# Kernel optimization log

Hardware: AMD Instinct MI355X
Metric: run time of the kernel (lower is better)

## Reference

```python
import jax, jax.numpy as jnp
import numpy as np

NUM_HEADS = 12


def setup_inputs() -> dict:
    key = jax.random.key(0)
    ks = jax.random.split(key, 8)
    B, D, H, W, C = 4, 8, 14, 14, 768
    hd = C // NUM_HEADS
    return {
        "x": jax.random.normal(ks[0], (B, D, H, W, C), jnp.float32),
        "qkv_w": jax.random.normal(ks[1], (C, 3 * C), jnp.float32) * (C ** -0.5),
        "qkv_b": jax.random.normal(ks[2], (3 * C,), jnp.float32) * 0.02,
        "proj_w": jax.random.normal(ks[3], (C, C), jnp.float32) * (C ** -0.5),
        "proj_b": jax.random.normal(ks[4], (C,), jnp.float32) * 0.02,
        "rel_pos_d": jax.random.normal(ks[5], (2 * D - 1, hd), jnp.float32) * 0.02,
        "rel_pos_h": jax.random.normal(ks[6], (2 * H - 1, hd), jnp.float32) * 0.02,
        "rel_pos_w": jax.random.normal(ks[7], (2 * W - 1, hd), jnp.float32) * 0.02,
    }


def _rel_table(table, n):
    # q_size == k_size == n; relative coords in [0, 2n-2]
    idx = jnp.arange(n)[:, None] - jnp.arange(n)[None, :] + (n - 1)
    return table[idx]  # [n, n, head_dim]


def reference(x, qkv_w, qkv_b, proj_w, proj_b, rel_pos_d, rel_pos_h, rel_pos_w):
    B, D, H, W, C = x.shape
    hd = C // NUM_HEADS
    scale = hd ** -0.5
    N = D * H * W
    BH = B * NUM_HEADS

    qkv = x @ qkv_w + qkv_b  # [B,D,H,W,3C]
    qkv = qkv.reshape(B, N, 3, NUM_HEADS, hd).transpose(2, 0, 3, 1, 4).reshape(3, BH, N, hd)
    q, k, v = qkv[0], qkv[1], qkv[2]

    attn = jnp.einsum('bnc,bmc->bnm', q * scale, k)  # [BH, N, N]

    # decomposed 3D relative position bias
    Rd = _rel_table(rel_pos_d, D)  # [D,D,hd]
    Rh = _rel_table(rel_pos_h, H)  # [H,H,hd]
    Rw = _rel_table(rel_pos_w, W)  # [W,W,hd]
    r_q = q.reshape(BH, D, H, W, hd)
    rel_d = jnp.einsum('bdhwc,dkc->bdhwk', r_q, Rd)  # [BH,D,H,W,D]
    rel_h = jnp.einsum('bdhwc,hkc->bdhwk', r_q, Rh)  # [BH,D,H,W,H]
    rel_w = jnp.einsum('bdhwc,wkc->bdhwk', r_q, Rw)  # [BH,D,H,W,W]
    attn = (attn.reshape(BH, D, H, W, D, H, W)
            + rel_d[:, :, :, :, :, None, None]
            + rel_h[:, :, :, :, None, :, None]
            + rel_w[:, :, :, :, None, None, :]).reshape(BH, N, N)

    attn = jax.nn.softmax(attn, axis=-1)
    out = jnp.einsum('bnm,bmc->bnc', attn, v)  # [BH,N,hd]
    out = out.reshape(B, NUM_HEADS, D, H, W, hd).transpose(0, 2, 3, 4, 1, 5).reshape(B, D, H, W, C)
    return out @ proj_w + proj_b
```

## Files before the change

kernel.cpp:

```cpp
#include <hip/hip_runtime.h>


typedef __bf16 bf16x8 __attribute__((ext_vector_type(8)));
typedef float f32x4 __attribute__((ext_vector_type(4)));

#define MFMA16(a, b, c) __builtin_amdgcn_mfma_f32_16x16x32_bf16((a), (b), (c), 0, 0, 0)

#if __has_builtin(__builtin_amdgcn_exp2f)
#define EXP2(x) __builtin_amdgcn_exp2f(x)
#else
#define EXP2(x) exp2f(x)
#endif

static __device__ __forceinline__ unsigned short f2bf(float f) {
    union { float f; unsigned int u; } v; v.f = f;
    unsigned int u = v.u;
    return (unsigned short)((u + 0x7fffu + ((u >> 16) & 1u)) >> 16);
}

static __device__ __forceinline__ bf16x8 ld_bf8(const unsigned short* p) {
    return *reinterpret_cast<const bf16x8*>(p);
}

static __device__ __forceinline__ void dma16(const void* g, void* l) {
    __builtin_amdgcn_global_load_lds(
        (const __attribute__((address_space(1))) void*)g,
        (__attribute__((address_space(3))) void*)l, 16, 0, 0);
}


static __device__ __forceinline__ void do_transpose(const float* __restrict__ w,
                                                    unsigned short* __restrict__ wt,
                                                    int K, int N, int bx, int by,
                                                    float (*tile)[65]) {
    int kt = bx * 64;
    int nt = by * 64;
    int tid = threadIdx.x;
    int r = tid >> 2;
    int cg = tid & 3;
#pragma unroll
    for (int i = 0; i < 4; ++i) {
        int c = cg * 16 + i * 4;
        float4 v = *reinterpret_cast<const float4*>(&w[(size_t)(kt + r) * N + nt + c]);
        tile[r][c + 0] = v.x; tile[r][c + 1] = v.y; tile[r][c + 2] = v.z; tile[r][c + 3] = v.w;
    }
    __syncthreads();
#pragma unroll
    for (int i = 0; i < 4; ++i) {
        int c = cg * 16 + i * 4;
        ushort4 o;
        o.x = f2bf(tile[c + 0][r]);
        o.y = f2bf(tile[c + 1][r]);
        o.z = f2bf(tile[c + 2][r]);
        o.w = f2bf(tile[c + 3][r]);
        *reinterpret_cast<ushort4*>(&wt[(size_t)(nt + r) * K + kt + c]) = o;
    }
}

__global__ __launch_bounds__(256) void k_prep(const float* __restrict__ x,
                                              unsigned short* __restrict__ xbf,
                                              const float* __restrict__ qkv_w,
                                              unsigned short* __restrict__ w1t,
                                              const float* __restrict__ proj_w,
                                              unsigned short* __restrict__ w2t,
                                              const float* __restrict__ rd,
                                              const float* __restrict__ rh,
                                              const float* __restrict__ rw,
                                              unsigned short* __restrict__ Tbf,
                                              unsigned short* __restrict__ indb) {
    __shared__ float tile[64][65];
    int bid = blockIdx.x;
    if (bid < 4704) {
        int i = bid * 256 + threadIdx.x;
        if (i < 1204224) {
            float4 v = reinterpret_cast<const float4*>(x)[i];
            ushort4 o;
            o.x = f2bf(v.x); o.y = f2bf(v.y); o.z = f2bf(v.z); o.w = f2bf(v.w);
            reinterpret_cast<ushort4*>(xbf)[i] = o;
        }
    } else if (bid < 5136) {
        int t = bid - 4704;
        do_transpose(qkv_w, w1t, 768, 2304, t % 12, t / 12, tile);
    } else if (bid < 5280) {
        int t = bid - 5136;
        do_transpose(proj_w, w2t, 768, 768, t % 12, t / 12, tile);
    } else if (bid < 5300) {
        int i = (bid - 5280) * 256 + threadIdx.x;
        if (i < 80 * 64) {
            int row = i >> 6, c = i & 63;
            float v = 0.f;
            if (row < 15) v = rd[row * 64 + c];
            else if (row < 42) v = rh[(row - 15) * 64 + c];
            else if (row < 69) v = rw[(row - 42) * 64 + c];
            Tbf[i] = f2bf(v * 1.44269504f);
        }
    } else {
        int i = (bid - 5300) * 256 + threadIdx.x;
        if (i < 1600 * 64) {
            int key = i >> 6, c = i & 63;
            unsigned short v = 0;
            if (key < 1568) {
                int kd = key / 196;
                int r = key - kd * 196;
                int kh = r / 14;
                int kw = r - kh * 14;
                if (c == kd || c == 8 + kh || c == 22 + kw) v = 0x3F80;
            } else {
                if (c == 36) v = 0x3F80;
            }
            indb[i] = v;
        }
    }
}

static __device__ __forceinline__ void gemm_core(const unsigned short* __restrict__ A,
                                                 const unsigned short* __restrict__ B,
                                                 int M_base, int N_base,
                                                 char* smem, f32x4 acc[4][4]) {
    const int lane = threadIdx.x & 63;
    const int wid = threadIdx.x >> 6;
    const int ww = wid & 1, wh = wid >> 1;
    const int quad = lane >> 4, l16 = lane & 15;
    const int sr = lane >> 3, sc = lane & 7;
    unsigned short* sA = (unsigned short*)smem;
    unsigned short* sB = (unsigned short*)(smem + 16384);

    for (int kt = 0; kt < 12; ++kt) {
#pragma unroll
        for (int j = 0; j < 4; ++j) {
            int loc = wid * 32 + j * 8 + sr;
            int gc = ((sc + loc) & 7) * 16;
            dma16((const char*)A + (size_t)(M_base + loc) * 1536 + kt * 128 + gc,
                  (char*)sA + (wid * 32 + j * 8) * 128);
            dma16((const char*)B + (size_t)(N_base + loc) * 1536 + kt * 128 + gc,
                  (char*)sB + (wid * 32 + j * 8) * 128);
        }
        __syncthreads();
#pragma unroll
        for (int s = 0; s < 2; ++s) {
            bf16x8 af[4], bfr[4];
#pragma unroll
            for (int i = 0; i < 4; ++i) {
                int ar = wh * 64 + i * 16 + l16;
                af[i] = ld_bf8(sA + ar * 64 + (((s * 4 + quad) - ar) & 7) * 8);
                int br = ww * 64 + i * 16 + l16;
                bfr[i] = ld_bf8(sB + br * 64 + (((s * 4 + quad) - br) & 7) * 8);
            }
#pragma unroll
            for (int i = 0; i < 4; ++i)
#pragma unroll
                for (int j2 = 0; j2 < 4; ++j2)
                    acc[i][j2] = MFMA16(af[i], bfr[j2], acc[i][j2]);
        }
        __syncthreads();
    }
}

static __device__ __forceinline__ void gemm_core64(const unsigned short* __restrict__ A,
                                                   const unsigned short* __restrict__ B,
                                                   int M_base, int N_base,
                                                   char* smem, f32x4 acc[4][2]) {
    const int lane = threadIdx.x & 63;
    const int wid = threadIdx.x >> 6;
    const int quad = lane >> 4, l16 = lane & 15;
    const int sr = lane >> 3, sc = lane & 7;
    unsigned short* sA = (unsigned short*)smem;
    unsigned short* sB = (unsigned short*)(smem + 8192);

    for (int kt = 0; kt < 12; ++kt) {
#pragma unroll
        for (int j = 0; j < 2; ++j) {
            int loc = wid * 16 + j * 8 + sr;
            int gc = ((sc + loc) & 7) * 16;
            dma16((const char*)A + (size_t)(M_base + loc) * 1536 + kt * 128 + gc,
                  (char*)sA + (wid * 16 + j * 8) * 128);
        }
#pragma unroll
        for (int j = 0; j < 4; ++j) {
            int loc = wid * 32 + j * 8 + sr;
            int gc = ((sc + loc) & 7) * 16;
            dma16((const char*)B + (size_t)(N_base + loc) * 1536 + kt * 128 + gc,
                  (char*)sB + (wid * 32 + j * 8) * 128);
        }
        __syncthreads();
#pragma unroll
        for (int s = 0; s < 2; ++s) {
            bf16x8 af[4], bfr[2];
#pragma unroll
            for (int i = 0; i < 4; ++i) {
                int ar = i * 16 + l16;
                af[i] = ld_bf8(sA + ar * 64 + (((s * 4 + quad) - ar) & 7) * 8);
            }
#pragma unroll
            for (int j = 0; j < 2; ++j) {
                int br = wid * 32 + j * 16 + l16;
                bfr[j] = ld_bf8(sB + br * 64 + (((s * 4 + quad) - br) & 7) * 8);
            }
#pragma unroll
            for (int i = 0; i < 4; ++i)
#pragma unroll
                for (int j = 0; j < 2; ++j)
                    acc[i][j] = MFMA16(af[i], bfr[j], acc[i][j]);
        }
        __syncthreads();
    }
}

__global__ __launch_bounds__(256, 4) void k_qkv(const unsigned short* __restrict__ xbf,
                                                const unsigned short* __restrict__ w1t,
                                                const float* __restrict__ qkv_b,
                                                unsigned short* __restrict__ qb,
                                                unsigned short* __restrict__ kb2,
                                                unsigned short* __restrict__ vb) {
    __shared__ __align__(16) char smem[32768];
    f32x4 acc[4][4] = {};
    gemm_core(xbf, w1t, blockIdx.x * 128, blockIdx.y * 128, smem, acc);

    const int lane = threadIdx.x & 63;
    const int wid = threadIdx.x >> 6;
    const int ww = wid & 1, wh = wid >> 1;
    const int quad = lane >> 4, l16 = lane & 15;
#pragma unroll
    for (int j = 0; j < 4; ++j) {
        int n = blockIdx.y * 128 + ww * 64 + j * 16 + l16;
        float bias = qkv_b[n];
        int which = n / 768;
        int rem = n - which * 768;
        int head = rem >> 6;
        int c = rem & 63;
#pragma unroll
        for (int i = 0; i < 4; ++i) {
#pragma unroll
            for (int r = 0; r < 4; ++r) {
                int m = blockIdx.x * 128 + wh * 64 + i * 16 + quad * 4 + r;
                float val = acc[i][j][r] + bias;
                int b_ = m / 1568;
                int nn = m - b_ * 1568;
                size_t idx = ((size_t)(b_ * 12 + head) * 1568 + nn) * 64 + c;
                if (which == 0)      qb[idx] = f2bf(val);
                else if (which == 1) kb2[(((size_t)(b_ * 12 + head)) * 1600 + nn) * 64 + c] = f2bf(val * 0.18033688f);
                else                 vb[idx] = f2bf(val);
            }
        }
    }
}

__global__ __launch_bounds__(256) void k_vt(const unsigned short* __restrict__ vb,
                                            unsigned short* __restrict__ vtb) {
    __shared__ unsigned short t[64][72];
    int bh = blockIdx.y;
    int n0 = blockIdx.x * 64;
    int tid = threadIdx.x;
    int r = tid >> 2, cg = (tid & 3) * 16;
    int n = n0 + r;
    if (n > 1567) n = 1567;
    const unsigned short* src = vb + ((size_t)bh * 1568 + n) * 64 + cg;
    *reinterpret_cast<uint4*>(&t[r][cg]) = *reinterpret_cast<const uint4*>(src);
    *reinterpret_cast<uint4*>(&t[r][cg + 8]) = *reinterpret_cast<const uint4*>(src + 8);
    __syncthreads();
    int c = tid >> 2, ng = (tid & 3) * 16;
    if (n0 + ng < 1568) {
        unsigned short buf[16];
#pragma unroll
        for (int i = 0; i < 16; ++i) buf[i] = t[ng + i][c];
        unsigned short* dst = vtb + ((size_t)bh * 64 + c) * 1600 + n0 + ng;
        *reinterpret_cast<uint4*>(dst) = *reinterpret_cast<uint4*>(&buf[0]);
        *reinterpret_cast<uint4*>(dst + 8) = *reinterpret_cast<uint4*>(&buf[8]);
    }
}

__global__ __launch_bounds__(256, 3) void k_attn(const unsigned short* __restrict__ qb,
                                                 const unsigned short* __restrict__ kb2,
                                                 const unsigned short* __restrict__ indb,
                                                 const unsigned short* __restrict__ vtb,
                                                 const unsigned short* __restrict__ Tbf,
                                                 unsigned short* __restrict__ obf) {
    __shared__ __align__(16) char smem[52224];
    const int lane = threadIdx.x & 63;
    const int wid = threadIdx.x >> 6;
    const int quad = lane >> 4;
    const int l16 = lane & 15;
    const int sr = lane >> 3;
    const int sc = lane & 7;
    const int bh = blockIdx.x;
    const int qt = blockIdx.y;

    unsigned short* pw = (unsigned short*)(smem + 43008 + wid * 2304);
    unsigned short* tR = (unsigned short*)(smem + wid * 5120);
    unsigned short* tB = (unsigned short*)(smem + 21504 + wid * 4608);

    const int iA = wid * 64 + lane;
    const int ioA = (iA / 5) * 128 + (iA % 5) * 16;
    const int iB = 256 + lane;
    const int ioB = (iB / 5) * 128 + (iB % 5) * 16;

    bf16x8 a_q0[2], a_q1[2], a_b0[2], a_b1[2];
#pragma unroll
    for (int mt = 0; mt < 2; ++mt) {
        int qrow = qt * 128 + wid * 32 + mt * 16 + l16;
        if (qrow > 1567) qrow = 1567;
        const unsigned short* qp = qb + ((size_t)bh * 1568 + qrow) * 64 + quad * 8;
        a_q0[mt] = ld_bf8(qp);
        a_q1[mt] = ld_bf8(qp + 32);
    }
#pragma unroll
    for (int mt = 0; mt < 2; ++mt) {
#pragma unroll
        for (int ng = 0; ng < 5; ++ng) {
            const unsigned short* tp = Tbf + (size_t)(ng * 16 + l16) * 64 + quad * 8;
            f32x4 t = {};
            t = MFMA16(a_q0[mt], ld_bf8(tp), t);
            t = MFMA16(a_q1[mt], ld_bf8(tp + 32), t);
#pragma unroll
            for (int r = 0; r < 4; ++r)
                tR[(mt * 16 + quad * 4 + r) * 80 + ng * 16 + l16] = f2bf(t[r]);
        }
    }
#pragma unroll
    for (int mt = 0; mt < 2; ++mt) {
        int gq = qt * 128 + wid * 32 + mt * 16 + l16;
        if (gq > 1567) gq = 1567;
        int qd = gq / 196;
        int rm = gq - qd * 196;
        int qh = rm / 14;
        int qw = rm - qh * 14;
        const unsigned short* qr = tR + (mt * 16 + l16) * 80;
        unsigned short* qxr = tB + (mt * 16 + l16) * 72;
#pragma unroll
        for (int t = 0; t < 16; ++t) {
            int dd = quad * 16 + t;
            unsigned short v = 0;
            if (dd < 8)        v = qr[qd - dd + 7];
            else if (dd < 22)  v = qr[15 + qh - (dd - 8) + 13];
            else if (dd < 36)  v = qr[42 + qw - (dd - 22) + 13];
            else if (dd == 36) v = 0xC6EA;
            qxr[dd] = v;
        }
    }
#pragma unroll
    for (int mt = 0; mt < 2; ++mt) {
        const unsigned short* qx = tB + (mt * 16 + l16) * 72;
        a_b0[mt] = ld_bf8(qx + quad * 8);
        a_b1[mt] = ld_bf8(qx + 32 + quad * 8);
    }
    __syncthreads();

    const char* kbh_b = (const char*)(kb2 + (size_t)bh * 1600 * 64);
    const char* ind_b = (const char*)indb;
    const char* vbh_b = (const char*)(vtb + (size_t)bh * 64 * 1600);

    auto stage = [&](char* sbase, int kb0) {
#pragma unroll
        for (int j = 0; j < 2; ++j) {
            int loc = wid * 16 + j * 8 + sr;
            int gc = ((sc + loc) & 7) * 16;
            dma16(kbh_b + (size_t)(kb0 + loc) * 128 + gc, sbase + (wid * 16 + j * 8) * 128);
            dma16(vbh_b + (size_t)loc * 3200 + (size_t)kb0 * 2 + gc,
                  sbase + 13312 + (wid * 16 + j * 8) * 128);
        }
        dma16(ind_b + (size_t)kb0 * 128 + ioA, sbase + 8192 + wid * 1024);
        if (wid == 0)
            dma16(ind_b + (size_t)kb0 * 128 + ioB, sbase + 8192 + 4096);
    };

    float l_p[2][4] = {};
    f32x4 Oacc[2][4] = {};

    stage(smem, 0);
    __syncthreads();

    for (int kt = 0; kt < 25; ++kt) {
        char* cur = smem + (kt & 1) * 21504;
        if (kt < 24) stage(smem + ((kt + 1) & 1) * 21504, (kt + 1) * 64);

        const unsigned short* sK = (const unsigned short*)cur;
        const unsigned short* sI = (const unsigned short*)(cur + 8192);
        const unsigned short* sV = (const unsigned short*)(cur + 13312);

        float p[2][4][4];
#pragma unroll
        for (int kg = 0; kg < 4; ++kg) {
            int key = kg * 16 + l16;
            const unsigned short* kr = sK + key * 64;
            bf16x8 bk0 = ld_bf8(kr + ((quad - key) & 7) * 8);
            bf16x8 bk1 = ld_bf8(kr + ((quad + 4 - key) & 7) * 8);
            const unsigned short* ir = sI + key * 40;
            bf16x8 bi0 = ld_bf8(ir + quad * 8);
            bf16x8 bi1 = ld_bf8(ir + 32 + quad * 8);
#pragma unroll
            for (int mt = 0; mt < 2; ++mt) {
                f32x4 t = {};
                t = MFMA16(a_q0[mt], bk0, t);
                t = MFMA16(a_q1[mt], bk1, t);
                t = MFMA16(a_b0[mt], bi0, t);
                t = MFMA16(a_b1[mt], bi1, t);
#pragma unroll
                for (int r = 0; r < 4; ++r) {
                    union { float f; unsigned int u; } c;
                    c.f = EXP2(t[r]);
                    c.u &= 0xFFFF0000u;
                    p[mt][kg][r] = c.f;
                    l_p[mt][r] += c.f;
                }
            }
        }
        bf16x8 v0[4], v1[4];
#pragma unroll
        for (int cg = 0; cg < 4; ++cg) {
            int dim = cg * 16 + l16;
            const unsigned short* vr = sV + dim * 64;
            v0[cg] = ld_bf8(vr + ((quad - dim) & 7) * 8);
            v1[cg] = ld_bf8(vr + ((quad + 4 - dim) & 7) * 8);
        }
#pragma unroll
        for (int mt = 0; mt < 2; ++mt) {
#pragma unroll
            for (int kg = 0; kg < 4; ++kg)
#pragma unroll
                for (int r = 0; r < 4; ++r) {
                    union { float f; unsigned int u; } c;
                    c.f = p[mt][kg][r];
                    pw[(quad * 4 + r) * 72 + kg * 16 + l16] = (unsigned short)(c.u >> 16);
                }
            const unsigned short* pr = pw + l16 * 72;
            bf16x8 ap0 = ld_bf8(pr + quad * 8);
            bf16x8 ap1 = ld_bf8(pr + 32 + quad * 8);
#pragma unroll
            for (int cg = 0; cg < 4; ++cg) {
                Oacc[mt][cg] = MFMA16(ap0, v0[cg], Oacc[mt][cg]);
                Oacc[mt][cg] = MFMA16(ap1, v1[cg], Oacc[mt][cg]);
            }
        }
        __syncthreads();
    }

    int b_ = bh / 12;
    int head = bh - b_ * 12;
    unsigned short* ob = obf + (size_t)b_ * 1568 * 768 + head * 64;
#pragma unroll
    for (int mt = 0; mt < 2; ++mt)
#pragma unroll
        for (int r = 0; r < 4; ++r) {
            float v = l_p[mt][r];
            v += __shfl_xor(v, 1);
            v += __shfl_xor(v, 2);
            v += __shfl_xor(v, 4);
            v += __shfl_xor(v, 8);
            int gq = qt * 128 + wid * 32 + mt * 16 + quad * 4 + r;
            if (gq < 1568) {
                float inv = 1.0f / v;
#pragma unroll
                for (int cg = 0; cg < 4; ++cg)
                    ob[(size_t)gq * 768 + cg * 16 + l16] = f2bf(Oacc[mt][cg][r] * inv);
            }
        }
}

__global__ __launch_bounds__(256, 4) void k_proj(const unsigned short* __restrict__ obf,
                                                 const unsigned short* __restrict__ w2t,
                                                 const float* __restrict__ proj_b,
                                                 float* __restrict__ out) {
    __shared__ __align__(16) char smem[24576];
    f32x4 acc[4][2] = {};
    gemm_core64(obf, w2t, blockIdx.x * 64, blockIdx.y * 128, smem, acc);

    const int lane = threadIdx.x & 63;
    const int wid = threadIdx.x >> 6;
    const int quad = lane >> 4, l16 = lane & 15;
#pragma unroll
    for (int j = 0; j < 2; ++j) {
        int n = blockIdx.y * 128 + wid * 32 + j * 16 + l16;
        float bias = proj_b[n];
#pragma unroll
        for (int i = 0; i < 4; ++i) {
#pragma unroll
            for (int r = 0; r < 4; ++r) {
                int m = blockIdx.x * 64 + i * 16 + quad * 4 + r;
                out[(size_t)m * 768 + n] = acc[i][j][r] + bias;
            }
        }
    }
}

extern "C" void kernel_launch(void* const* d_in, const int* in_sizes, int n_in,
                              void* d_out, int out_size, void* d_ws, size_t ws_size,
                              hipStream_t stream) {
    const float* x      = (const float*)d_in[0];
    const float* qkv_w  = (const float*)d_in[1];
    const float* qkv_b  = (const float*)d_in[2];
    const float* proj_w = (const float*)d_in[3];
    const float* proj_b = (const float*)d_in[4];
    const float* rd     = (const float*)d_in[5];
    const float* rh     = (const float*)d_in[6];
    const float* rw     = (const float*)d_in[7];
    float* out = (float*)d_out;

    char* ws = (char*)d_ws;
    size_t off = 0;
    auto alloc = [&](size_t bytes) {
        char* p = ws + off;
        off += (bytes + 255) & ~(size_t)255;
        return p;
    };
    unsigned short* xbf  = (unsigned short*)alloc((size_t)6272 * 768 * 2);
    unsigned short* w1t  = (unsigned short*)alloc((size_t)2304 * 768 * 2);
    unsigned short* w2t  = (unsigned short*)alloc((size_t)768 * 768 * 2);
    unsigned short* Tbf  = (unsigned short*)alloc((size_t)80 * 64 * 2);
    unsigned short* qb   = (unsigned short*)alloc((size_t)48 * 1568 * 64 * 2);
    unsigned short* kb2  = (unsigned short*)alloc((size_t)48 * 1600 * 64 * 2);
    unsigned short* vtb  = (unsigned short*)alloc((size_t)48 * 64 * 1600 * 2);
    unsigned short* indb = (unsigned short*)alloc((size_t)1600 * 64 * 2);
    unsigned short* obf  = xbf;
    unsigned short* vb   = (unsigned short*)d_out;

    hipLaunchKernelGGL(k_prep, dim3(5700), dim3(256), 0, stream,
                       x, xbf, qkv_w, w1t, proj_w, w2t, rd, rh, rw, Tbf, indb);
    hipLaunchKernelGGL(k_qkv, dim3(49, 18), dim3(256), 0, stream, xbf, w1t, qkv_b, qb, kb2, vb);
    hipLaunchKernelGGL(k_vt, dim3(25, 48), dim3(256), 0, stream, vb, vtb);
    hipLaunchKernelGGL(k_attn, dim3(48, 13), dim3(256), 0, stream, qb, kb2, indb, vtb, Tbf, obf);
    hipLaunchKernelGGL(k_proj, dim3(98, 6), dim3(256), 0, stream, obf, w2t, proj_b, out);
}
```

Measured before the change: 226.6 us.

## Fuse V transpose into QKV GEMM epilogue and drop separate transpose kernel

Blocks of the QKV GEMM that produce V now stage their bf16 output tile in shared memory. They then write it directly in the transposed [bh, c, n] layout that the attention kernel consumes. This removes the intermediate V buffer round-trip through global memory and one kernel launch. The cost is slightly more shared memory, extra barriers in the V blocks, and 16-byte strided stores with a large stride.

```diff
diff --git a/kernel.cpp b/kernel.cpp
--- a/kernel.cpp
+++ b/kernel.cpp
@@ -211,8 +211,8 @@
                                                 const float* __restrict__ qkv_b,
                                                 unsigned short* __restrict__ qb,
                                                 unsigned short* __restrict__ kb2,
-                                                unsigned short* __restrict__ vb) {
-    __shared__ __align__(16) char smem[32768];
+                                                unsigned short* __restrict__ vtb) {
+    __shared__ __align__(16) char smem[36864];
     f32x4 acc[4][4] = {};
     gemm_core(xbf, w1t, blockIdx.x * 128, blockIdx.y * 128, smem, acc);
 
@@ -220,52 +220,61 @@
     const int wid = threadIdx.x >> 6;
     const int ww = wid & 1, wh = wid >> 1;
     const int quad = lane >> 4, l16 = lane & 15;
-#pragma unroll
-    for (int j = 0; j < 4; ++j) {
-        int n = blockIdx.y * 128 + ww * 64 + j * 16 + l16;
-        float bias = qkv_b[n];
-        int which = n / 768;
-        int rem = n - which * 768;
-        int head = rem >> 6;
-        int c = rem & 63;
-#pragma unroll
-        for (int i = 0; i < 4; ++i) {
-#pragma unroll
-            for (int r = 0; r < 4; ++r) {
-                int m = blockIdx.x * 128 + wh * 64 + i * 16 + quad * 4 + r;
-                float val = acc[i][j][r] + bias;
-                int b_ = m / 1568;
-                int nn = m - b_ * 1568;
-                size_t idx = ((size_t)(b_ * 12 + head) * 1568 + nn) * 64 + c;
-                if (which == 0)      qb[idx] = f2bf(val);
-                else if (which == 1) kb2[(((size_t)(b_ * 12 + head)) * 1600 + nn) * 64 + c] = f2bf(val * 0.18033688f);
-                else                 vb[idx] = f2bf(val);
-            }
-        }
-    }
-}
-
-__global__ __launch_bounds__(256) void k_vt(const unsigned short* __restrict__ vb,
-                                            unsigned short* __restrict__ vtb) {
-    __shared__ unsigned short t[64][72];
-    int bh = blockIdx.y;
-    int n0 = blockIdx.x * 64;
-    int tid = threadIdx.x;
-    int r = tid >> 2, cg = (tid & 3) * 16;
-    int n = n0 + r;
-    if (n > 1567) n = 1567;
-    const unsigned short* src = vb + ((size_t)bh * 1568 + n) * 64 + cg;
-    *reinterpret_cast<uint4*>(&t[r][cg]) = *reinterpret_cast<const uint4*>(src);
-    *reinterpret_cast<uint4*>(&t[r][cg + 8]) = *reinterpret_cast<const uint4*>(src + 8);
-    __syncthreads();
-    int c = tid >> 2, ng = (tid & 3) * 16;
-    if (n0 + ng < 1568) {
-        unsigned short buf[16];
-#pragma unroll
-        for (int i = 0; i < 16; ++i) buf[i] = t[ng + i][c];
-        unsigned short* dst = vtb + ((size_t)bh * 64 + c) * 1600 + n0 + ng;
-        *reinterpret_cast<uint4*>(dst) = *reinterpret_cast<uint4*>(&buf[0]);
-        *reinterpret_cast<uint4*>(dst + 8) = *reinterpret_cast<uint4*>(&buf[8]);
+    const int which = blockIdx.y / 6;
+
+    if (which < 2) {
+#pragma unroll
+        for (int j = 0; j < 4; ++j) {
+            int n = blockIdx.y * 128 + ww * 64 + j * 16 + l16;
+            float bias = qkv_b[n];
+            int rem = n - which * 768;
+            int head = rem >> 6;
+            int c = rem & 63;
+#pragma unroll
+            for (int i = 0; i < 4; ++i) {
+#pragma unroll
+                for (int r = 0; r < 4; ++r) {
+                    int m = blockIdx.x * 128 + wh * 64 + i * 16 + quad * 4 + r;
+                    float val = acc[i][j][r] + bias;
+                    int b_ = m / 1568;
+                    int nn = m - b_ * 1568;
+                    if (which == 0)
+                        qb[((size_t)(b_ * 12 + head) * 1568 + nn) * 64 + c] = f2bf(val);
+                    else
+                        kb2[((size_t)(b_ * 12 + head) * 1600 + nn) * 64 + c] = f2bf(val * 0.18033688f);
+                }
+            }
+        }
+    } else {
+        unsigned short (*tile)[132] = (unsigned short (*)[132])smem;
+        __syncthreads();
+#pragma unroll
+        for (int j = 0; j < 4; ++j) {
+            int n = blockIdx.y * 128 + ww * 64 + j * 16 + l16;
+            float bias = qkv_b[n];
+#pragma unroll
+            for (int i = 0; i < 4; ++i)
+#pragma unroll
+                for (int r = 0; r < 4; ++r)
+                    tile[wh * 64 + i * 16 + quad * 4 + r][ww * 64 + j * 16 + l16] =
+                        f2bf(acc[i][j][r] + bias);
+        }
+        __syncthreads();
+        int nl = threadIdx.x >> 1;
+        int mh = (threadIdx.x & 1) * 64;
+        int rem = blockIdx.y * 128 - 1536 + nl;
+        int head = rem >> 6, c = rem & 63;
+#pragma unroll
+        for (int k8 = 0; k8 < 64; k8 += 8) {
+            int m8 = blockIdx.x * 128 + mh + k8;
+            int b_ = m8 / 1568;
+            int nn = m8 - b_ * 1568;
+            unsigned short buf[8];
+#pragma unroll
+            for (int t = 0; t < 8; ++t) buf[t] = tile[mh + k8 + t][nl];
+            *reinterpret_cast<uint4*>(vtb + ((size_t)(b_ * 12 + head) * 64 + c) * 1600 + nn) =
+                *reinterpret_cast<uint4*>(buf);
+        }
     }
 }
 
@@ -511,12 +520,10 @@
     unsigned short* vtb  = (unsigned short*)alloc((size_t)48 * 64 * 1600 * 2);
     unsigned short* indb = (unsigned short*)alloc((size_t)1600 * 64 * 2);
     unsigned short* obf  = xbf;
-    unsigned short* vb   = (unsigned short*)d_out;
 
     hipLaunchKernelGGL(k_prep, dim3(5700), dim3(256), 0, stream,
                        x, xbf, qkv_w, w1t, proj_w, w2t, rd, rh, rw, Tbf, indb);
-    hipLaunchKernelGGL(k_qkv, dim3(49, 18), dim3(256), 0, stream, xbf, w1t, qkv_b, qb, kb2, vb);
-    hipLaunchKernelGGL(k_vt, dim3(25, 48), dim3(256), 0, stream, vb, vtb);
+    hipLaunchKernelGGL(k_qkv, dim3(49, 18), dim3(256), 0, stream, xbf, w1t, qkv_b, qb, kb2, vtb);
     hipLaunchKernelGGL(k_attn, dim3(48, 13), dim3(256), 0, stream, qb, kb2, indb, vtb, Tbf, obf);
     hipLaunchKernelGGL(k_proj, dim3(98, 6), dim3(256), 0, stream, obf, w2t, proj_b, out);
 }
```

Result: faster. 221.1 us (-2.5%).
